# Optimization experiments

Measured on AMD Instinct MI355X. Metric: run time of the kernel, lower is better.

## Reference

```python
import math
import jax, jax.numpy as jnp
import numpy as np

L_LAYERS, H, D, DV, DM, LMAX, V = 4, 16, 1024, 64, 4096, 1024, 32000


def setup_inputs() -> dict:
    key = jax.random.key(0)
    ks = iter(jax.random.split(key, 40))
    def rn(shape, s=0.02):
        return jax.random.normal(next(ks), shape, jnp.float32) * s
    x_ids = jax.random.randint(next(ks), (LMAX,), 0, V)
    return dict(
        x_ids=x_ids,
        word_emb=rn((V, D)), pos_emb=rn((LMAX, D)),
        Wq=rn((L_LAYERS, H, D, D)), bq=jnp.zeros((L_LAYERS, H, D), jnp.float32),
        Wk=rn((L_LAYERS, H, D, D)), bk=jnp.zeros((L_LAYERS, H, D), jnp.float32),
        Wv=rn((L_LAYERS, H, D, DV)), bv=jnp.zeros((L_LAYERS, H, DV), jnp.float32),
        Wo=rn((L_LAYERS, H * DV, D)), bo=jnp.zeros((L_LAYERS, D), jnp.float32),
        g1=rn((L_LAYERS, D), 0.01), b1=rn((L_LAYERS, D), 0.01),
        g2=rn((L_LAYERS, D), 0.01), b2=rn((L_LAYERS, D), 0.01),
        W1=rn((L_LAYERS, D, DM)), bm1=jnp.zeros((L_LAYERS, DM), jnp.float32),
        W2=rn((L_LAYERS, DM, D)), bm2=jnp.zeros((L_LAYERS, D), jnp.float32),
        gf=rn((D,), 0.01), bf=rn((D,), 0.01),
        Wu=rn((D, V)), bu=jnp.zeros((V,), jnp.float32),
    )


def _ln(x, g, b):
    # original normalizes each row over the full embedding vector (biased std)
    mu = jnp.mean(x, axis=-1, keepdims=True)
    sd = jnp.sqrt(jnp.mean((x - mu) ** 2, axis=-1, keepdims=True))
    return g * (x - mu) / sd + b


def reference(x_ids, word_emb, pos_emb, Wq, bq, Wk, bk, Wv, bv, Wo, bo,
              g1, b1, g2, b2, W1, bm1, W2, bm2, gf, bf, Wu, bu):
    x = word_emb[x_ids] + pos_emb[jnp.arange(LMAX)]          # (LMAX, D)
    mask = jnp.tril(jnp.ones((LMAX, LMAX), bool))
    scale = 1.0 / math.sqrt(D)                               # d_attn = d_e
    for l in range(L_LAYERS):
        xn = _ln(x, g1[l], b1[l])
        q = jnp.einsum('ld,hde->hle', xn, Wq[l]) + bq[l][:, None, :]
        k = jnp.einsum('ld,hde->hle', xn, Wk[l]) + bk[l][:, None, :]
        v = jnp.einsum('ld,hdv->hlv', xn, Wv[l]) + bv[l][:, None, :]
        s = jnp.einsum('hqe,hke->hqk', q, k)                 # (H, LMAX, LMAX)
        s = jnp.where(mask, s, -jnp.inf)
        a = jax.nn.softmax(s * scale, axis=-1)
        o = jnp.einsum('hqk,hkv->hqv', a, v)                 # (H, LMAX, DV)
        # faithful reproduction of MHAttention's OVERLAPPING slice writes:
        # head h writes columns [h, h+DV), later heads overwrite earlier ones
        y = jnp.zeros((LMAX, H * DV), x.dtype)
        for h in range(H):
            y = y.at[:, h:h + DV].set(o[h])
        x = x + y @ Wo[l] + bo[l]
        xn2 = _ln(x, g2[l], b2[l])
        # x + act_layer(xn2) where act_layer(z) = z + mlp2(gelu(mlp1(z)))
        x = x + xn2 + jax.nn.gelu(xn2 @ W1[l] + bm1[l]) @ W2[l] + bm2[l]
    x = _ln(x, gf, bf)
    return jax.nn.softmax(x @ Wu + bu, axis=-1)              # (LMAX, V)
```

## Files before the change

### kernel.cpp

```cpp
#include <hip/hip_runtime.h>

typedef __bf16 bf16_t;
typedef __bf16 bf16x8 __attribute__((ext_vector_type(8)));
typedef float f32x4 __attribute__((ext_vector_type(4)));
typedef unsigned int u32;

#define SEQ    1024
#define DEMB   1024
#define NHEAD  16
#define DVDIM  64
#define DMLP   4096
#define NVOCAB 32000
#define NLAYER 4

typedef const __attribute__((address_space(1))) void gas_t;
typedef __attribute__((address_space(3))) void las_t;

__device__ __forceinline__ void gload_lds16(const void* g, void* l) {
  __builtin_amdgcn_global_load_lds((gas_t*)g, (las_t*)l, 16, 0, 0);
}

union PackU { bf16_t h[2]; u32 u; };
union B4U  { uint2 u; bf16_t h[4]; };

__device__ __forceinline__ float blockSum(float v, float* red) {
  #pragma unroll
  for (int o = 32; o > 0; o >>= 1) v += __shfl_down(v, o, 64);
  __syncthreads();
  if ((threadIdx.x & 63) == 0) red[threadIdx.x >> 6] = v;
  __syncthreads();
  return (red[0] + red[1]) + (red[2] + red[3]);
}
__device__ __forceinline__ float blockMax(float v, float* red) {
  #pragma unroll
  for (int o = 32; o > 0; o >>= 1) v = fmaxf(v, __shfl_down(v, o, 64));
  __syncthreads();
  if ((threadIdx.x & 63) == 0) red[threadIdx.x >> 6] = v;
  __syncthreads();
  return fmaxf(fmaxf(red[0], red[1]), fmaxf(red[2], red[3]));
}

__device__ __forceinline__ void ln_body(float4 v, const float* __restrict__ g,
                                        const float* __restrict__ b,
                                        bf16_t* __restrict__ xn, int row, int t,
                                        float* red, float* xupd_row) {
  float mu = blockSum(v.x + v.y + v.z + v.w, red) * (1.0f / DEMB);
  float dx = v.x - mu, dy = v.y - mu, dz = v.z - mu, dw = v.w - mu;
  float var = blockSum(dx * dx + dy * dy + dz * dz + dw * dw, red) * (1.0f / DEMB);
  float inv = 1.0f / sqrtf(var);
  float4 gv = *(const float4*)(g + t * 4);
  float4 bv = *(const float4*)(b + t * 4);
  float o0 = gv.x * dx * inv + bv.x;
  float o1 = gv.y * dy * inv + bv.y;
  float o2 = gv.z * dz * inv + bv.z;
  float o3 = gv.w * dw * inv + bv.w;
  PackU p0, p1;
  p0.h[0] = (bf16_t)o0; p0.h[1] = (bf16_t)o1;
  p1.h[0] = (bf16_t)o2; p1.h[1] = (bf16_t)o3;
  uint2 st; st.x = p0.u; st.y = p1.u;
  *(uint2*)(xn + (long)row * DEMB + t * 4) = st;
  if (xupd_row) {
    float4 nv; nv.x = v.x + o0; nv.y = v.y + o1; nv.z = v.z + o2; nv.w = v.w + o3;
    *(float4*)(xupd_row + t * 4) = nv;
  }
}

__global__ void __launch_bounds__(256)
embedln_k(const int* __restrict__ ids, const float* __restrict__ we,
          const float* __restrict__ pe, const float* __restrict__ g,
          const float* __restrict__ b, float* __restrict__ x,
          bf16_t* __restrict__ xn) {
  __shared__ float red[4];
  const int row = blockIdx.x, t = threadIdx.x;
  const long id = ids[row];
  float4 a = *(const float4*)(we + id * (long)DEMB + t * 4);
  float4 p = *(const float4*)(pe + (long)row * DEMB + t * 4);
  float4 v; v.x = a.x + p.x; v.y = a.y + p.y; v.z = a.z + p.z; v.w = a.w + p.w;
  *(float4*)(x + (long)row * DEMB + t * 4) = v;
  ln_body(v, g, b, xn, row, t, red, nullptr);
}

__global__ void __launch_bounds__(256)
ln_k(const float* __restrict__ x, const float* __restrict__ g,
     const float* __restrict__ b, bf16_t* __restrict__ xn,
     float* __restrict__ xupd) {
  __shared__ float red[4];
  const int row = blockIdx.x, t = threadIdx.x;
  float4 v = *(const float4*)(x + (long)row * DEMB + t * 4);
  ln_body(v, g, b, xn, row, t, red, xupd ? xupd + (long)row * DEMB : nullptr);
}

__global__ void __launch_bounds__(256)
redln_k(const float* __restrict__ P, const float* __restrict__ bm2,
        float* __restrict__ X, const float* __restrict__ g,
        const float* __restrict__ b, bf16_t* __restrict__ xn) {
  __shared__ float red[4];
  const int row = blockIdx.x, t = threadIdx.x;
  const long i = (long)row * 1024 + t * 4;
  float4 x = *(float4*)(X + i);
  #pragma unroll
  for (int z = 0; z < 4; ++z) {
    float4 p = *(const float4*)(P + (long)z * 1048576 + i);
    x.x += p.x; x.y += p.y; x.z += p.z; x.w += p.w;
  }
  float4 bb = *(const float4*)(bm2 + t * 4);
  x.x += bb.x; x.y += bb.y; x.z += bb.z; x.w += bb.w;
  *(float4*)(X + i) = x;
  ln_body(x, g, b, xn, row, t, red, nullptr);
}

__global__ void biascat_k(const float* __restrict__ bq, const float* __restrict__ bk,
                          float* __restrict__ out) {
  const int z = blockIdx.x, t = threadIdx.x;
  const int l = z >> 5, i = z & 31;
  const float* src = (i < NHEAD) ? (bq + (long)(l * NHEAD + i) * DEMB)
                                 : (bk + (long)(l * NHEAD + i - NHEAD) * DEMB);
  *(float4*)(out + (long)z * DEMB + t * 4) = *(const float4*)(src + t * 4);
}

__global__ void zyb_k(bf16_t* __restrict__ y) {
  *(uint4*)((char*)y + ((long)blockIdx.x * 256 + threadIdx.x) * 16) = uint4{0, 0, 0, 0};
}

__device__ __forceinline__ void tconv_tile(const float* __restrict__ ip,
                                           bf16_t* __restrict__ op,
                                           int R, int C, int rx, int ry,
                                           float (*tf)[65]) {
  const int c0 = rx * 64, r0 = ry * 64;
  const int t = threadIdx.x;
  const int lr = t >> 4, lc = (t & 15) * 4;
  #pragma unroll
  for (int p = 0; p < 4; ++p) {
    const float4 v = *(const float4*)(ip + (long)(r0 + lr + 16 * p) * C + (c0 + lc));
    tf[lr + 16 * p][lc + 0] = v.x;
    tf[lr + 16 * p][lc + 1] = v.y;
    tf[lr + 16 * p][lc + 2] = v.z;
    tf[lr + 16 * p][lc + 3] = v.w;
  }
  __syncthreads();
  const int j = t & 7;
  const int n = t >> 3;
  #pragma unroll
  for (int p = 0; p < 2; ++p) {
    const int nn = n + 32 * p;
    u32 w[4];
    #pragma unroll
    for (int q = 0; q < 4; ++q) {
      PackU u;
      u.h[0] = (bf16_t)tf[j * 8 + 2 * q][nn];
      u.h[1] = (bf16_t)tf[j * 8 + 2 * q + 1][nn];
      w[q] = u.u;
    }
    *(uint4*)(op + (long)(c0 + nn) * R + (r0 + j * 8)) = *(uint4*)&w[0];
  }
}

__global__ void __launch_bounds__(256)
tconvall_k(const float* __restrict__ Wq, const float* __restrict__ Wk,
           const float* __restrict__ Wv, const float* __restrict__ Wo,
           const float* __restrict__ W1, const float* __restrict__ W2,
           const float* __restrict__ Wu,
           bf16_t* __restrict__ WTqk, bf16_t* __restrict__ WTv,
           bf16_t* __restrict__ WTo, bf16_t* __restrict__ WT1,
           bf16_t* __restrict__ WT2, bf16_t* __restrict__ WTu) {
  __shared__ float tf[64][65];
  const long DD = (long)DEMB * DEMB;
  const int b = blockIdx.x;
  const float* ip; bf16_t* op; int R, C, rx, ry;
  if (b < 32768) {
    const int z = b >> 8, rem = b & 255; ry = rem >> 4; rx = rem & 15;
    R = 1024; C = 1024;
    const int l = z >> 5, i = z & 31;
    ip = (i < NHEAD) ? (Wq + (long)(l * NHEAD + i) * DD)
                     : (Wk + (long)(l * NHEAD + i - NHEAD) * DD);
    op = WTqk + (long)z * DD;
  } else if (b < 33792) {
    const int idx = b - 32768; const int z = idx >> 4; ry = idx & 15; rx = 0;
    R = 1024; C = 64;
    ip = Wv + (long)z * 65536; op = WTv + (long)z * 65536;
  } else if (b < 33920) {
    const int idx = b - 33792; const int z = idx >> 5; ry = (idx >> 4) & 1; rx = idx & 15;
    R = 128; C = 1024;
    ip = Wo + (long)z * DD; op = WTo + (long)z * 131072;
  } else if (b < 38016) {
    const int idx = b - 33920; const int z = idx >> 10; ry = (idx >> 6) & 15; rx = idx & 63;
    R = 1024; C = 4096;
    ip = W1 + (long)z * 4194304; op = WT1 + (long)z * 4194304;
  } else if (b < 42112) {
    const int idx = b - 38016; const int z = idx >> 10; ry = (idx >> 4) & 63; rx = idx & 15;
    R = 4096; C = 1024;
    ip = W2 + (long)z * 4194304; op = WT2 + (long)z * 4194304;
  } else {
    const int idx = b - 42112; ry = idx / 500; rx = idx - ry * 500;
    R = 1024; C = 32000;
    ip = Wu; op = WTu;
  }
  tconv_tile(ip, op, R, C, rx, ry, tf);
}

template<int MODE, int BN, bool CAUSAL, bool TRIMK>
__global__ void __launch_bounds__(256)
gemm_k(const bf16_t* __restrict__ A, const bf16_t* __restrict__ B,
       const float* __restrict__ bias, void* __restrict__ Cv,
       int M, int N, int K, int lda, int ldb,
       long aB, long bB, long cB, int biasB) {
  __shared__ bf16_t lsA[128 * 32];
  __shared__ bf16_t lsB[BN * 32];

  const int t = threadIdx.x;
  const int bz = blockIdx.z;
  const int m0 = blockIdx.y * 128;
  const int n0 = blockIdx.x * BN;
  if (CAUSAL && n0 > m0 + 127) return;

  const bf16_t* Ap = A + (long)bz * aB;
  const bf16_t* Bp = B + (long)bz * bB;
  const int kEnd = TRIMK ? min(K, m0 + 128) : K;

  constexpr int NS = BN / 32;
  const int lane = t & 63;
  const int wid = t >> 6;
  const int wr = (wid >> 1) * 64;
  const int wc = (wid & 1) * (BN / 2);
  const int fr = lane & 15, fg = lane >> 4;
  const int srow = lane >> 2;
  const int skc  = (lane & 3) * 8;

  f32x4 acc[4][NS] = {};

  for (int k0 = 0; k0 < kEnd; k0 += 32) {
    if (k0) __syncthreads();
    #pragma unroll
    for (int i = 0; i < 2; ++i) {
      const int seg = wid * 2 + i;
      gload_lds16(Ap + (long)(m0 + seg * 16 + srow) * lda + (k0 + skc),
                  lsA + seg * 512);
    }
    if (BN == 128) {
      #pragma unroll
      for (int i = 0; i < 2; ++i) {
        const int seg = wid * 2 + i;
        gload_lds16(Bp + (long)(n0 + seg * 16 + srow) * ldb + (k0 + skc),
                    lsB + seg * 512);
      }
    } else {
      gload_lds16(Bp + (long)(n0 + wid * 16 + srow) * ldb + (k0 + skc),
                  lsB + wid * 512);
    }
    __syncthreads();

    bf16x8 af[4], bfv[NS];
    #pragma unroll
    for (int ms = 0; ms < 4; ++ms)
      af[ms] = *(const bf16x8*)(lsA + (wr + ms * 16 + fr) * 32 + fg * 8);
    #pragma unroll
    for (int ns = 0; ns < NS; ++ns)
      bfv[ns] = *(const bf16x8*)(lsB + (wc + ns * 16 + fr) * 32 + fg * 8);
    #pragma unroll
    for (int ms = 0; ms < 4; ++ms)
      #pragma unroll
      for (int ns = 0; ns < NS; ++ns)
        acc[ms][ns] = __builtin_amdgcn_mfma_f32_16x16x32_bf16(
            af[ms], bfv[ns], acc[ms][ns], 0, 0, 0);
  }

  #pragma unroll
  for (int ms = 0; ms < 4; ++ms) {
    #pragma unroll
    for (int ns = 0; ns < NS; ++ns) {
      const int col = n0 + wc + ns * 16 + fr;
      const float bvv = bias ? bias[(long)bz * biasB + col] : 0.0f;
      #pragma unroll
      for (int r = 0; r < 4; ++r) {
        const int row = m0 + wr + ms * 16 + fg * 4 + r;
        float v = acc[ms][ns][r] + bvv;
        if (MODE == 1) {
          ((float*)Cv)[(long)bz * cB + (long)row * N + col] += v;
        } else if (MODE == 2) {
          ((float*)Cv)[(long)bz * cB + (long)row * N + col] = v;
        } else if (MODE == 3) {
          float gl = 0.5f * v * (1.0f + tanhf(0.7978845608028654f * (v + 0.044715f * v * v * v)));
          ((bf16_t*)Cv)[(long)bz * cB + (long)row * N + col] = (bf16_t)gl;
        } else {
          if (bz == NHEAD - 1) {
            ((bf16_t*)Cv)[(long)row * 128 + (NHEAD - 1) + col] = (bf16_t)v;
          } else if (col == 0) {
            ((bf16_t*)Cv)[(long)row * 128 + bz] = (bf16_t)v;
          }
        }
      }
    }
  }
}

#define GPHASE(buf, mh, nh, STAGE, VM) do {                                            \
  bf16x8 af[4][2], bfv[2][2];                                                          \
  _Pragma("unroll") for (int mf = 0; mf < 4; ++mf) {                                   \
    const int r = wm * 128 + ((mh) * 4 + mf) * 16 + (lane & 15);                       \
    _Pragma("unroll") for (int ks = 0; ks < 2; ++ks) {                                 \
      const int slot = ks * 4 + (lane >> 4);                                           \
      af[mf][ks] = *(const bf16x8*)(lds + (buf) * 32768 + r * 64 +                     \
                                    ((slot ^ (r & 7)) << 3)); } }                      \
  _Pragma("unroll") for (int nf = 0; nf < 2; ++nf) {                                   \
    const int r = wn * 64 + ((nh) * 2 + nf) * 16 + (lane & 15);                        \
    _Pragma("unroll") for (int ks = 0; ks < 2; ++ks) {                                 \
      const int slot = ks * 4 + (lane >> 4);                                           \
      bfv[nf][ks] = *(const bf16x8*)(lds + (buf) * 32768 + 16384 + r * 64 +            \
                                     ((slot ^ (r & 7)) << 3)); } }                     \
  STAGE;                                                                               \
  __builtin_amdgcn_s_barrier();                                                        \
  asm volatile("s_waitcnt lgkmcnt(0)" ::: "memory");                                   \
  __builtin_amdgcn_sched_barrier(0);                                                   \
  __builtin_amdgcn_s_setprio(1);                                                       \
  _Pragma("unroll") for (int mf = 0; mf < 4; ++mf)                                     \
    _Pragma("unroll") for (int nf = 0; nf < 2; ++nf)                                   \
      _Pragma("unroll") for (int ks = 0; ks < 2; ++ks)                                 \
        acc[(mh) * 4 + mf][(nh) * 2 + nf] = __builtin_amdgcn_mfma_f32_16x16x32_bf16(   \
            af[mf][ks], bfv[nf][ks], acc[(mh) * 4 + mf][(nh) * 2 + nf], 0, 0, 0);      \
  __builtin_amdgcn_s_setprio(0);                                                       \
  VM;                                                                                  \
  __builtin_amdgcn_s_barrier();                                                        \
} while (0)

template<int MODE, bool CAUSAL, bool HASV>
__global__ void __launch_bounds__(512, 1)
gemm256_k(const bf16_t* __restrict__ A, const bf16_t* __restrict__ B,
          const float* __restrict__ bias, void* __restrict__ Cv,
          int M, int N, int K, long aB, long bB, long cB, int biasB,
          const bf16_t* __restrict__ B2, const float* __restrict__ bias2,
          bf16_t* __restrict__ Cv2) {
  __shared__ bf16_t lds[65536];

  const int t = threadIdx.x;
  const int lane = t & 63, w = t >> 6;
  const int wm = w >> 2, wn = w & 3;
  const int bz = blockIdx.z;
  const int m0 = blockIdx.y * 256, n0 = blockIdx.x * 256;
  if (CAUSAL && n0 > m0 + 255) return;

  const bool vm = HASV && (bz == 32);
  const bf16_t* Ap = A + (long)bz * aB;
  const bf16_t* Bp = vm ? B2 : B + (long)bz * bB;
  const int NT = K >> 6;

  f32x4 acc[8][4] = {};

  auto stA = [&](int half, int kt, int buf) {
    #pragma unroll
    for (int rr = 0; rr < 2; ++rr) {
      const int rw0 = rr * 64 + w * 8;
      const int row0 = ((rw0 >> 6) << 7) | (half << 6) | (rw0 & 63);
      const int r = row0 + (lane >> 3);
      const int slot = lane & 7;
      gload_lds16(Ap + (long)(m0 + r) * K + (kt << 6) + ((slot ^ (r & 7)) << 3),
                  lds + buf * 32768 + row0 * 64);
    }
  };
  auto stB = [&](int half, int kt, int buf) {
    #pragma unroll
    for (int rr = 0; rr < 2; ++rr) {
      const int rw0 = rr * 64 + w * 8;
      const int row0 = ((rw0 >> 5) << 6) | (half << 5) | (rw0 & 31);
      const int r = row0 + (lane >> 3);
      const int slot = lane & 7;
      gload_lds16(Bp + (long)(n0 + r) * K + (kt << 6) + ((slot ^ (r & 7)) << 3),
                  lds + buf * 32768 + 16384 + row0 * 64);
    }
  };

  stB(0, 0, 0); stA(0, 0, 0); stA(1, 0, 0); stB(1, 0, 0);
  stB(0, 1, 1); stA(0, 1, 1);
  asm volatile("s_waitcnt vmcnt(4)" ::: "memory");
  __builtin_amdgcn_s_barrier();

  for (int it = 0; it < (NT >> 1); ++it) {
    const int tt = it * 2;
    const int s1 = min(tt + 1, NT - 1);
    const int s2 = min(tt + 2, NT - 1);
    const int s3 = min(tt + 3, NT - 1);
    GPHASE(0, 0, 0, { stA(1, s1, 1); }, );
    GPHASE(0, 1, 0, { stB(1, s1, 1); }, );
    GPHASE(0, 0, 1, { stB(0, s2, 0); }, );
    GPHASE(0, 1, 1, { stA(0, s2, 0); }, asm volatile("s_waitcnt vmcnt(4)" ::: "memory"));
    GPHASE(1, 0, 0, { stA(1, s2, 0); }, );
    GPHASE(1, 1, 0, { stB(1, s2, 0); }, );
    GPHASE(1, 0, 1, { stB(0, s3, 1); }, );
    GPHASE(1, 1, 1, { stA(0, s3, 1); }, asm volatile("s_waitcnt vmcnt(4)" ::: "memory"));
  }
  asm volatile("s_waitcnt vmcnt(0)" ::: "memory");

  #pragma unroll
  for (int mf = 0; mf < 8; ++mf) {
    #pragma unroll
    for (int nf = 0; nf < 4; ++nf) {
      const int col = n0 + wn * 64 + nf * 16 + (lane & 15);
      const int row0 = m0 + wm * 128 + mf * 16 + (lane >> 4) * 4;
      if (HASV && vm) {
        const float bvv = bias2[col];
        PackU p0, p1;
        p0.h[0] = (bf16_t)(acc[mf][nf][0] + bvv);
        p0.h[1] = (bf16_t)(acc[mf][nf][1] + bvv);
        p1.h[0] = (bf16_t)(acc[mf][nf][2] + bvv);
        p1.h[1] = (bf16_t)(acc[mf][nf][3] + bvv);
        uint2 st; st.x = p0.u; st.y = p1.u;
        *(uint2*)(Cv2 + (long)col * M + row0) = st;
      } else {
        const float bvv = bias ? bias[(long)bz * biasB + col] : 0.0f;
        #pragma unroll
        for (int r = 0; r < 4; ++r) {
          const float v = acc[mf][nf][r] + bvv;
          if (MODE == 0)
            ((bf16_t*)Cv)[(long)bz * cB + (long)(row0 + r) * N + col] = (bf16_t)v;
          else
            ((float*)Cv)[(long)bz * cB + (long)(row0 + r) * N + col] = v;
        }
      }
    }
  }
}

__global__ void __launch_bounds__(256)
smax_k(bf16_t* __restrict__ s) {
  __shared__ float red[4];
  const int q = blockIdx.x, h = blockIdx.y, t = threadIdx.x;
  bf16_t* sr = s + ((long)h * SEQ + q) * SEQ;
  const int L = q + 1;
  const float scale = 0.03125f;
  B4U b; b.u = *(const uint2*)(sr + t * 4);
  float x[4];
  float m = -1e30f;
  #pragma unroll
  for (int j = 0; j < 4; ++j) {
    x[j] = (float)b.h[j] * scale;
    if (t * 4 + j < L) m = fmaxf(m, x[j]);
  }
  m = blockMax(m, red);
  float e[4], sum = 0.0f;
  #pragma unroll
  for (int j = 0; j < 4; ++j) {
    e[j] = (t * 4 + j < L) ? expf(x[j] - m) : 0.0f;
    sum += e[j];
  }
  __syncthreads();
  sum = blockSum(sum, red);
  const float inv = 1.0f / sum;
  #pragma unroll
  for (int j = 0; j < 4; ++j) b.h[j] = (bf16_t)(e[j] * inv);
  *(uint2*)(sr + t * 4) = b.u;
}

__global__ void __launch_bounds__(1024)
vsmax_k(float* __restrict__ out) {
  __shared__ float rm[16], rs[16];
  const int row = blockIdx.x, t = threadIdx.x;
  float* r = out + (long)row * NVOCAB;
  float v[32];
  const int nlast = (t < NVOCAB - 31 * 1024) ? 32 : 31;
  float m = -1e30f;
  #pragma unroll
  for (int j = 0; j < 31; ++j) { v[j] = r[j * 1024 + t]; m = fmaxf(m, v[j]); }
  if (nlast == 32) { v[31] = r[31 * 1024 + t]; m = fmaxf(m, v[31]); } else v[31] = -1e30f;
  float s = 0.0f;
  #pragma unroll
  for (int j = 0; j < 32; ++j) s += expf(v[j] - m);
  #pragma unroll
  for (int o = 32; o > 0; o >>= 1) {
    const float mo = __shfl_down(m, o, 64);
    const float so = __shfl_down(s, o, 64);
    const float M2 = fmaxf(m, mo);
    s = s * expf(m - M2) + so * expf(mo - M2);
    m = M2;
  }
  if ((t & 63) == 0) { rm[t >> 6] = m; rs[t >> 6] = s; }
  __syncthreads();
  float M = -1e30f;
  #pragma unroll
  for (int i = 0; i < 16; ++i) M = fmaxf(M, rm[i]);
  float S = 0.0f;
  #pragma unroll
  for (int i = 0; i < 16; ++i) S += rs[i] * expf(rm[i] - M);
  const float inv = 1.0f / S;
  #pragma unroll
  for (int j = 0; j < 31; ++j) r[j * 1024 + t] = expf(v[j] - M) * inv;
  if (nlast == 32) r[31 * 1024 + t] = expf(v[31] - M) * inv;
}

extern "C" void kernel_launch(void* const* d_in, const int* in_sizes, int n_in,
                              void* d_out, int out_size, void* d_ws, size_t ws_size,
                              hipStream_t stream) {
  (void)in_sizes; (void)n_in; (void)out_size; (void)ws_size;
  const int*   x_ids = (const int*)  d_in[0];
  const float* wemb  = (const float*)d_in[1];
  const float* pemb  = (const float*)d_in[2];
  const float* Wq    = (const float*)d_in[3];
  const float* bq    = (const float*)d_in[4];
  const float* Wk    = (const float*)d_in[5];
  const float* bk    = (const float*)d_in[6];
  const float* Wv    = (const float*)d_in[7];
  const float* bv    = (const float*)d_in[8];
  const float* Wo    = (const float*)d_in[9];
  const float* bo    = (const float*)d_in[10];
  const float* g1    = (const float*)d_in[11];
  const float* b1    = (const float*)d_in[12];
  const float* g2    = (const float*)d_in[13];
  const float* b2    = (const float*)d_in[14];
  const float* W1    = (const float*)d_in[15];
  const float* bm1   = (const float*)d_in[16];
  const float* W2    = (const float*)d_in[17];
  const float* bm2   = (const float*)d_in[18];
  const float* gf    = (const float*)d_in[19];
  const float* bfin  = (const float*)d_in[20];
  const float* Wu    = (const float*)d_in[21];
  const float* bu    = (const float*)d_in[22];

  char* ws = (char*)d_ws;
  float*  X    = (float*) ws;
  bf16_t* ACT  = (bf16_t*)(ws + (4u   << 20));
  bf16_t* VbT  = (bf16_t*)(ws + (6u   << 20));
  bf16_t* Yb   = (bf16_t*)(ws + (10u  << 20));
  bf16_t* H1   = (bf16_t*)(ws + (12u  << 20));
  bf16_t* QKb  = (bf16_t*)(ws + (20u  << 20));
  float*  PART = (float*) (ws + (84u  << 20));
  float*  BIAS = (float*) (ws + (100u << 20));
  bf16_t* WTqk = (bf16_t*)(ws + (128u << 20));
  bf16_t* WTv  = (bf16_t*)(ws + (384u << 20));
  bf16_t* WTo  = (bf16_t*)(ws + (392u << 20));
  bf16_t* WT1  = (bf16_t*)(ws + (400u << 20));
  bf16_t* WT2  = (bf16_t*)(ws + (432u << 20));
  bf16_t* WTu  = (bf16_t*)(ws + (464u << 20));

  bf16_t* Sb  = (bf16_t*)d_out;
  float*  OUT = (float*)d_out;

  const long DD = (long)DEMB * DEMB;
  const long SD = (long)SEQ * DEMB;

  embedln_k<<<SEQ, 256, 0, stream>>>(x_ids, wemb, pemb, g1, b1, X, ACT);
  biascat_k<<<128, 256, 0, stream>>>(bq, bk, BIAS);
  zyb_k<<<64, 256, 0, stream>>>(Yb);
  tconvall_k<<<50112, 256, 0, stream>>>(Wq, Wk, Wv, Wo, W1, W2, Wu,
                                        WTqk, WTv, WTo, WT1, WT2, WTu);

  for (int l = 0; l < NLAYER; ++l) {
    gemm256_k<0, false, true><<<dim3(4, 4, 33), 512, 0, stream>>>(
        ACT, WTqk + (long)l * 32 * DD, BIAS + (long)l * 32 * DEMB, QKb,
        SEQ, DEMB, DEMB, 0L, DD, SD, DEMB,
        WTv + (long)l * DD, bv + (long)l * NHEAD * DVDIM, VbT);

    gemm256_k<0, true, false><<<dim3(4, 4, NHEAD), 512, 0, stream>>>(
        QKb, QKb + (long)NHEAD * SD, nullptr, Sb,
        SEQ, SEQ, DEMB, SD, SD, (long)SEQ * SEQ, 0, nullptr, nullptr, nullptr);
    smax_k<<<dim3(SEQ, NHEAD), 256, 0, stream>>>(Sb);

    gemm_k<6, 64, false, true><<<dim3(1, 8, NHEAD), 256, 0, stream>>>(
        Sb, VbT, nullptr, Yb,
        SEQ, DVDIM, SEQ, SEQ, SEQ, (long)SEQ * SEQ, (long)DVDIM * SEQ, 0L, 0);

    gemm_k<1, 128, false, false><<<dim3(8, 8, 1), 256, 0, stream>>>(
        Yb, WTo + (long)l * DEMB * 128, bo + (long)l * DEMB, X,
        SEQ, DEMB, 128, 128, 128, 0L, 0L, 0L, 0);

    ln_k<<<SEQ, 256, 0, stream>>>(X, g2 + l * DEMB, b2 + l * DEMB, ACT, X);

    gemm_k<3, 128, false, false><<<dim3(32, 8, 1), 256, 0, stream>>>(
        ACT, WT1 + (long)l * DMLP * DEMB, bm1 + (long)l * DMLP, H1,
        SEQ, DMLP, DEMB, DEMB, DEMB, 0L, 0L, 0L, 0);
    gemm_k<2, 128, false, false><<<dim3(8, 8, 4), 256, 0, stream>>>(
        H1, WT2 + (long)l * DEMB * DMLP, nullptr, PART,
        SEQ, DEMB, 1024, DMLP, DMLP, 1024L, 1024L, (long)SEQ * DEMB, 0);
    if (l < NLAYER - 1)
      redln_k<<<SEQ, 256, 0, stream>>>(PART, bm2 + (long)l * DEMB, X,
                                       g1 + (l + 1) * DEMB, b1 + (l + 1) * DEMB, ACT);
    else
      redln_k<<<SEQ, 256, 0, stream>>>(PART, bm2 + (long)l * DEMB, X, gf, bfin, ACT);
  }

  gemm256_k<2, false, false><<<dim3(125, 4, 1), 512, 0, stream>>>(
      ACT, WTu, bu, OUT, SEQ, NVOCAB, DEMB, 0L, 0L, 0L, 0,
      nullptr, nullptr, nullptr);
  vsmax_k<<<SEQ, 1024, 0, stream>>>(OUT);
}
```

Measured before the change: 1.540 ms.

## Fold first-column PV products into softmax; run full PV only for last head

Because of the overlapping slice writes, heads 0..14 contribute only their first output column. The softmax kernel now computes that single dot product of probabilities with the first V column and writes it to Y. The full P·V GEMM runs only for the last head. The bias-concat and Y-zero kernels are merged into one launch, and the output-projection GEMM uses a 64-wide N tile with twice as many blocks. This removes most of the P·V GEMM work for 15 heads, at the cost of an extra block reduction in softmax.

```diff
diff --git a/kernel.cpp b/kernel.cpp
--- a/kernel.cpp
+++ b/kernel.cpp
@@ -109,17 +109,17 @@
   ln_body(x, g, b, xn, row, t, red, nullptr);
 }
 
-__global__ void biascat_k(const float* __restrict__ bq, const float* __restrict__ bk,
-                          float* __restrict__ out) {
+__global__ void biaszyb_k(const float* __restrict__ bq, const float* __restrict__ bk,
+                          float* __restrict__ out, bf16_t* __restrict__ y) {
   const int z = blockIdx.x, t = threadIdx.x;
-  const int l = z >> 5, i = z & 31;
-  const float* src = (i < NHEAD) ? (bq + (long)(l * NHEAD + i) * DEMB)
-                                 : (bk + (long)(l * NHEAD + i - NHEAD) * DEMB);
-  *(float4*)(out + (long)z * DEMB + t * 4) = *(const float4*)(src + t * 4);
-}
-
-__global__ void zyb_k(bf16_t* __restrict__ y) {
-  *(uint4*)((char*)y + ((long)blockIdx.x * 256 + threadIdx.x) * 16) = uint4{0, 0, 0, 0};
+  if (z < 128) {
+    const int l = z >> 5, i = z & 31;
+    const float* src = (i < NHEAD) ? (bq + (long)(l * NHEAD + i) * DEMB)
+                                   : (bk + (long)(l * NHEAD + i - NHEAD) * DEMB);
+    *(float4*)(out + (long)z * DEMB + t * 4) = *(const float4*)(src + t * 4);
+  } else {
+    *(uint4*)((char*)y + ((long)(z - 128) * 256 + t) * 16) = uint4{0, 0, 0, 0};
+  }
 }
 
 __device__ __forceinline__ void tconv_tile(const float* __restrict__ ip,
@@ -282,11 +282,7 @@
           float gl = 0.5f * v * (1.0f + tanhf(0.7978845608028654f * (v + 0.044715f * v * v * v)));
           ((bf16_t*)Cv)[(long)bz * cB + (long)row * N + col] = (bf16_t)gl;
         } else {
-          if (bz == NHEAD - 1) {
-            ((bf16_t*)Cv)[(long)row * 128 + (NHEAD - 1) + col] = (bf16_t)v;
-          } else if (col == 0) {
-            ((bf16_t*)Cv)[(long)row * 128 + bz] = (bf16_t)v;
-          }
+          ((bf16_t*)Cv)[(long)row * 128 + 15 + col] = (bf16_t)v;
         }
       }
     }
@@ -420,7 +416,8 @@
 }
 
 __global__ void __launch_bounds__(256)
-smax_k(bf16_t* __restrict__ s) {
+smax_k(bf16_t* __restrict__ s, const bf16_t* __restrict__ V,
+       bf16_t* __restrict__ Yb) {
   __shared__ float red[4];
   const int q = blockIdx.x, h = blockIdx.y, t = threadIdx.x;
   bf16_t* sr = s + ((long)h * SEQ + q) * SEQ;
@@ -447,6 +444,15 @@
   #pragma unroll
   for (int j = 0; j < 4; ++j) b.h[j] = (bf16_t)(e[j] * inv);
   *(uint2*)(sr + t * 4) = b.u;
+  if (h != NHEAD - 1) {
+    const bf16_t* vc = V + (long)h * 64 * SEQ;
+    B4U vv; vv.u = *(const uint2*)(vc + t * 4);
+    float d = 0.0f;
+    #pragma unroll
+    for (int j = 0; j < 4; ++j) d += e[j] * (float)vv.h[j];
+    d = blockSum(d, red);
+    if (t == 0) Yb[(long)q * 128 + h] = (bf16_t)(d * inv);
+  }
 }
 
 __global__ void __launch_bounds__(1024)
@@ -536,8 +542,7 @@
   const long SD = (long)SEQ * DEMB;
 
   embedln_k<<<SEQ, 256, 0, stream>>>(x_ids, wemb, pemb, g1, b1, X, ACT);
-  biascat_k<<<128, 256, 0, stream>>>(bq, bk, BIAS);
-  zyb_k<<<64, 256, 0, stream>>>(Yb);
+  biaszyb_k<<<192, 256, 0, stream>>>(bq, bk, BIAS, Yb);
   tconvall_k<<<50112, 256, 0, stream>>>(Wq, Wk, Wv, Wo, W1, W2, Wu,
                                         WTqk, WTv, WTo, WT1, WT2, WTu);
 
@@ -550,13 +555,12 @@
     gemm256_k<0, true, false><<<dim3(4, 4, NHEAD), 512, 0, stream>>>(
         QKb, QKb + (long)NHEAD * SD, nullptr, Sb,
         SEQ, SEQ, DEMB, SD, SD, (long)SEQ * SEQ, 0, nullptr, nullptr, nullptr);
-    smax_k<<<dim3(SEQ, NHEAD), 256, 0, stream>>>(Sb);
-
-    gemm_k<6, 64, false, true><<<dim3(1, 8, NHEAD), 256, 0, stream>>>(
-        Sb, VbT, nullptr, Yb,
-        SEQ, DVDIM, SEQ, SEQ, SEQ, (long)SEQ * SEQ, (long)DVDIM * SEQ, 0L, 0);
-
-    gemm_k<1, 128, false, false><<<dim3(8, 8, 1), 256, 0, stream>>>(
+    smax_k<<<dim3(SEQ, NHEAD), 256, 0, stream>>>(Sb, VbT, Yb);
+    gemm_k<7, 64, false, true><<<dim3(1, 8, 1), 256, 0, stream>>>(
+        Sb + (long)(NHEAD - 1) * SEQ * SEQ, VbT + (long)(NHEAD - 1) * DVDIM * SEQ,
+        nullptr, Yb, SEQ, DVDIM, SEQ, SEQ, SEQ, 0L, 0L, 0L, 0);
+
+    gemm_k<1, 64, false, false><<<dim3(16, 8, 1), 256, 0, stream>>>(
         Yb, WTo + (long)l * DEMB * 128, bo + (long)l * DEMB, X,
         SEQ, DEMB, 128, 128, 128, 0L, 0L, 0L, 0);
 
```

After: 1.510 ms. About the same (-1.9%).
